# Performance work log

Hardware: AMD Instinct MI355X
Metric: run time of the kernel (lower is better)

## Reference

```python
import jax, jax.numpy as jnp
import numpy as np

DECAY = 0.99


def setup_inputs() -> dict:
    key = jax.random.key(0)
    k1, k2, k3, k4 = jax.random.split(key, 4)
    N, D, K = 65536, 256, 1024
    return {
        "masked_z_e_x": jax.random.normal(k1, (N, D), dtype=jnp.float32),
        "z_e_x": jax.random.normal(k2, (N, D), dtype=jnp.float32),
        "embedding": jax.random.normal(k3, (K, D), dtype=jnp.float32) * (1.0 / K),
        "ema_count": jnp.ones((K,), dtype=jnp.float32),
        "ema_w": jax.random.normal(k4, (K, D), dtype=jnp.float32) * (1.0 / K),
    }


def _vq_indices(x_flat, codebook):
    # distances[n,k] = ||x_n||^2 + ||c_k||^2 - 2 x_n . c_k  (addmm in torch)
    c_sqr = jnp.sum(codebook * codebook, axis=1)              # [K]
    x_sqr = jnp.sum(x_flat * x_flat, axis=1, keepdims=True)   # [N,1]
    dists = x_sqr + c_sqr - 2.0 * (x_flat @ codebook.T)       # [N,K]
    return jnp.argmin(dists, axis=1)                          # [N]


def reference(masked_z_e_x, z_e_x, embedding, ema_count, ema_w):
    K, D = embedding.shape
    x_flat = masked_z_e_x.reshape(-1, D)
    indices = _vq_indices(x_flat, embedding)                  # [N] int

    # straight-through quantized codes (value = gathered codes)
    z_q_x = embedding[indices].reshape(masked_z_e_x.shape)

    # EMA codebook update (training branch); one-hot matmul == segment sums
    z_flat = z_e_x.reshape(-1, D)
    counts = jax.ops.segment_sum(jnp.ones_like(indices, dtype=jnp.float32),
                                 indices, num_segments=K)     # [K]
    dw = jax.ops.segment_sum(z_flat, indices, num_segments=K) # [K,D]
    ema_count_new = DECAY * ema_count + (1.0 - DECAY) * counts
    ema_w_new = DECAY * ema_w + (1.0 - DECAY) * dw
    embedding_new = ema_w_new / ema_count_new[:, None]

    # re-gather from the updated (detached) codebook
    z_q_x_bar = embedding_new[indices].reshape(z_e_x.shape)
    return (z_q_x, z_q_x_bar, embedding_new, ema_count_new, ema_w_new)
```

## Files before the change

### kernel.cpp

```cpp
#include <hip/hip_runtime.h>

#define DDIM 256
#define KCODES 1024
#define MARGIN 2.0e-4f

typedef __attribute__((ext_vector_type(8))) short fragA;
typedef __attribute__((ext_vector_type(4))) float f32x4;

static __device__ __forceinline__ float4 ld4(const float* p) {
    return *reinterpret_cast<const float4*>(p);
}

static __device__ __forceinline__ ushort bf16_rne(float f) {
    unsigned bits = __float_as_uint(f);
    unsigned r = bits + 0x7FFFu + ((bits >> 16) & 1u);
    return (ushort)(r >> 16);
}

__global__ void split_sqnorm_kernel(const float* __restrict__ X, ushort* __restrict__ Xs,
                                    float* __restrict__ out, int nrows) {
    int row = blockIdx.x * 4 + (threadIdx.x >> 6);
    if (row >= nrows) return;
    int lane = threadIdx.x & 63;
    float4 v = reinterpret_cast<const float4*>(X + (size_t)row * DDIM)[lane];
    double s = (double)v.x * v.x + (double)v.y * v.y + (double)v.z * v.z + (double)v.w * v.w;
    #pragma unroll
    for (int off = 32; off > 0; off >>= 1) s += __shfl_down(s, off);
    if (lane == 0) out[row] = (float)s;

    float fv[4] = {v.x, v.y, v.z, v.w};
    ushort hb[4], lb[4];
    #pragma unroll
    for (int i = 0; i < 4; i++) {
        hb[i] = bf16_rne(fv[i]);
        float hf = __uint_as_float((unsigned)hb[i] << 16);
        lb[i] = bf16_rne(fv[i] - hf);
    }
    ushort4 hi = make_ushort4(hb[0], hb[1], hb[2], hb[3]);
    ushort4 lo = make_ushort4(lb[0], lb[1], lb[2], lb[3]);
    *reinterpret_cast<ushort4*>(Xs + (size_t)row * 512 + lane * 4) = hi;
    *reinterpret_cast<ushort4*>(Xs + (size_t)row * 512 + 256 + lane * 4) = lo;
}

__global__ __launch_bounds__(256) void argmin_mfma_kernel(
        const float* __restrict__ X, const ushort* __restrict__ Cs,
        float* __restrict__ xsq, const float* __restrict__ csq,
        int* __restrict__ indices, int* __restrict__ flag_cnt,
        int* __restrict__ flag_list, int* __restrict__ counts, int nrows_total) {
    __shared__ ushort clds[32 * 512];

    int tid = threadIdx.x;
    int w = tid >> 6;
    int l = tid & 63;
    int lm = l & 15;
    int lg = l >> 4;
    int row0 = blockIdx.x * 64;

    const float* xrowf = X + (size_t)(row0 + w * 16 + lm) * DDIM;
    fragA a_hi[8], a_lo[8];
    double dsum = 0.0;
    #pragma unroll
    for (int s = 0; s < 8; s++) {
        float4 v0 = ld4(xrowf + s * 32 + lg * 8);
        float4 v1 = ld4(xrowf + s * 32 + lg * 8 + 4);
        float f[8] = {v0.x, v0.y, v0.z, v0.w, v1.x, v1.y, v1.z, v1.w};
        fragA h, lo;
        #pragma unroll
        for (int j = 0; j < 8; j++) {
            dsum += (double)f[j] * f[j];
            ushort hb = bf16_rne(f[j]);
            float hf = __uint_as_float((unsigned)hb << 16);
            ushort lb = bf16_rne(f[j] - hf);
            h[j] = (short)hb;
            lo[j] = (short)lb;
        }
        a_hi[s] = h;
        a_lo[s] = lo;
    }
    dsum += __shfl_xor(dsum, 16);
    dsum += __shfl_xor(dsum, 32);
    float xsqf = (float)dsum;
    if (l < 16) xsq[row0 + w * 16 + l] = xsqf;
    float xs_r[4];
    #pragma unroll
    for (int r = 0; r < 4; r++) xs_r[r] = __shfl(xsqf, lg * 4 + r);

    float d1[4], d2[4];
    int k1[4];
    #pragma unroll
    for (int r = 0; r < 4; r++) { d1[r] = 3.0e38f; d2[r] = 3.0e38f; k1[r] = 0; }

    for (int kc = 0; kc < KCODES; kc += 32) {
        __syncthreads();
        #pragma unroll
        for (int it = 0; it < 8; it++) {
            int c = it * 256 + tid;
            int r = c >> 6, col = c & 63;
            int p = (col & 32) | ((col & 31) ^ (r & 7));
            *reinterpret_cast<float4*>(&clds[r * 512 + p * 8]) =
                *reinterpret_cast<const float4*>(Cs + (size_t)(kc + r) * 512 + col * 8);
        }
        __syncthreads();

        f32x4 acc[2];
        #pragma unroll
        for (int kt = 0; kt < 2; kt++) acc[kt] = (f32x4){0.f, 0.f, 0.f, 0.f};

        #pragma unroll
        for (int s = 0; s < 8; s++) {
            #pragma unroll
            for (int kt = 0; kt < 2; kt++) {
                int kl = kt * 16 + lm;
                int chi = (4 * s + lg) ^ (kl & 7);
                fragA bhi = *reinterpret_cast<const fragA*>(&clds[kl * 512 + chi * 8]);
                fragA blo = *reinterpret_cast<const fragA*>(&clds[kl * 512 + (32 + chi) * 8]);
                acc[kt] = __builtin_amdgcn_mfma_f32_16x16x32_bf16(a_hi[s], bhi, acc[kt], 0, 0, 0);
                acc[kt] = __builtin_amdgcn_mfma_f32_16x16x32_bf16(a_lo[s], bhi, acc[kt], 0, 0, 0);
                acc[kt] = __builtin_amdgcn_mfma_f32_16x16x32_bf16(a_hi[s], blo, acc[kt], 0, 0, 0);
            }
        }

        #pragma unroll
        for (int kt = 0; kt < 2; kt++) {
            int k = kc + kt * 16 + lm;
            float cs = csq[k];
            #pragma unroll
            for (int r = 0; r < 4; r++) {
                float dist = (xs_r[r] + cs) - 2.0f * acc[kt][r];
                if (dist < d1[r] || (dist == d1[r] && k < k1[r])) {
                    d2[r] = d1[r]; d1[r] = dist; k1[r] = k;
                } else if (dist < d2[r]) {
                    d2[r] = dist;
                }
            }
        }
    }

    #pragma unroll
    for (int r = 0; r < 4; r++) {
        float bd1 = d1[r], bd2 = d2[r];
        int bk1 = k1[r];
        #pragma unroll
        for (int m = 1; m < 16; m <<= 1) {
            float od1 = __shfl_xor(bd1, m);
            int ok1 = __shfl_xor(bk1, m);
            float od2 = __shfl_xor(bd2, m);
            if (od1 < bd1 || (od1 == bd1 && ok1 < bk1)) {
                bd2 = fminf(bd1, od2); bd1 = od1; bk1 = ok1;
            } else {
                bd2 = fminf(bd2, od1);
            }
        }
        if (lm == 0) {
            int row = row0 + w * 16 + lg * 4 + r;
            indices[row] = bk1;
            atomicAdd(&counts[bk1], 1);
            if (bd2 - bd1 < MARGIN) {
                int pos = atomicAdd(flag_cnt, 1);
                if (pos < nrows_total) flag_list[pos] = row;
            }
        }
    }
}

#define ECH 64
#define NKCH (KCODES / ECH)

__global__ __launch_bounds__(256) void exact_chunk_kernel(
        const float* __restrict__ X, const float* __restrict__ C,
        const float* __restrict__ xsq, const float* __restrict__ csq,
        const int* __restrict__ flag_cnt, const int* __restrict__ flag_list,
        unsigned long long* __restrict__ best64, int nrows_total) {
    __shared__ float xt[64][36];
    __shared__ float ct[64][36];
    __shared__ int rowidx[64];
    __shared__ float xsql[64];

    int cnt = *flag_cnt;
    if (cnt > nrows_total) cnt = nrows_total;
    if (cnt <= 0) return;
    int ntiles = (cnt + 63) >> 6;
    int nunits = ntiles * NKCH;

    int tid = threadIdx.x;
    int tx = tid & 15;
    int ty = tid >> 4;

    for (int u = blockIdx.x; u < nunits; u += gridDim.x) {
        int t = u >> 4;
        int kc = (u & 15) * ECH;
        int base = t * 64;

        __syncthreads();
        if (tid < 64) {
            int p = base + tid;
            int row = flag_list[p < cnt ? p : base];
            rowidx[tid] = row;
            xsql[tid] = xsq[row];
        }
        __syncthreads();

        float xs[4];
        #pragma unroll
        for (int i = 0; i < 4; i++) xs[i] = xsql[i * 16 + ty];

        float acc[4][4];
        #pragma unroll
        for (int i = 0; i < 4; i++)
            #pragma unroll
            for (int j = 0; j < 4; j++) acc[i][j] = 0.0f;

        for (int dt = 0; dt < DDIM; dt += 32) {
            __syncthreads();
            #pragma unroll
            for (int it = 0; it < 2; it++) {
                int e = it * 256 + tid;
                int r = e >> 3, c4 = e & 7;
                *reinterpret_cast<float4*>(&xt[r][c4 * 4]) =
                    ld4(X + (size_t)rowidx[r] * DDIM + dt + c4 * 4);
            }
            #pragma unroll
            for (int it = 0; it < 2; it++) {
                int e = it * 256 + tid;
                int r = e >> 3, c4 = e & 7;
                *reinterpret_cast<float4*>(&ct[r][c4 * 4]) =
                    ld4(C + (size_t)(kc + r) * DDIM + dt + c4 * 4);
            }
            __syncthreads();

            for (int d4 = 0; d4 < 32; d4 += 4) {
                float4 xv[4], cv[4];
                #pragma unroll
                for (int i = 0; i < 4; i++)
                    xv[i] = *reinterpret_cast<const float4*>(&xt[i * 16 + ty][d4]);
                #pragma unroll
                for (int j = 0; j < 4; j++)
                    cv[j] = *reinterpret_cast<const float4*>(&ct[j * 16 + tx][d4]);
                #pragma unroll
                for (int i = 0; i < 4; i++)
                    #pragma unroll
                    for (int j = 0; j < 4; j++) {
                        float a = acc[i][j];
                        a += xv[i].x * cv[j].x; a += xv[i].y * cv[j].y;
                        a += xv[i].z * cv[j].z; a += xv[i].w * cv[j].w;
                        acc[i][j] = a;
                    }
            }
        }

        float cs_r[4];
        #pragma unroll
        for (int j = 0; j < 4; j++) cs_r[j] = csq[kc + j * 16 + tx];

        #pragma unroll
        for (int i = 0; i < 4; i++) {
            float bd = 3.0e38f; int bk = 0;
            #pragma unroll
            for (int j = 0; j < 4; j++) {
                int kk = kc + j * 16 + tx;
                float tt = xs[i] + cs_r[j];
                float dist = tt - 2.0f * acc[i][j];
                if (dist < bd || (dist == bd && kk < bk)) { bd = dist; bk = kk; }
            }
            #pragma unroll
            for (int m = 1; m < 16; m <<= 1) {
                float od = __shfl_xor(bd, m);
                int ok = __shfl_xor(bk, m);
                if (od < bd || (od == bd && ok < bk)) { bd = od; bk = ok; }
            }
            if (tx == 0) {
                int p = base + i * 16 + ty;
                if (p < cnt) {
                    unsigned long long pk =
                        ((unsigned long long)__float_as_uint(bd) << 32) | (unsigned)bk;
                    atomicMin(&best64[p], pk);
                }
            }
        }
    }
}

__global__ void exact_finalize_kernel(const int* __restrict__ flag_cnt,
                                      const int* __restrict__ flag_list,
                                      const unsigned long long* __restrict__ best64,
                                      int* __restrict__ indices, int* __restrict__ counts,
                                      int nrows_total) {
    int cnt = *flag_cnt;
    if (cnt > nrows_total) cnt = nrows_total;
    for (int i = blockIdx.x * 256 + threadIdx.x; i < cnt; i += gridDim.x * 256) {
        int row = flag_list[i];
        int newk = (int)(best64[i] & 0xFFFFFFFFULL);
        int oldk = indices[row];
        if (newk != oldk) {
            indices[row] = newk;
            atomicAdd(&counts[oldk], -1);
            atomicAdd(&counts[newk], 1);
        }
    }
}

__global__ void prefix_kernel(const int* __restrict__ counts, int* __restrict__ offs,
                              int* __restrict__ cursor) {
    __shared__ int a[KCODES];
    int t = threadIdx.x;
    int v = counts[t];
    a[t] = v;
    __syncthreads();
    for (int s = 1; s < KCODES; s <<= 1) {
        int x = (t >= s) ? a[t - s] : 0;
        __syncthreads();
        a[t] += x;
        __syncthreads();
    }
    int excl = a[t] - v;
    offs[t] = excl;
    cursor[t] = excl;
}

__global__ void scatter_pos_kernel(const int* __restrict__ idx, int* __restrict__ cursor,
                                   int* __restrict__ sorted) {
    int i = blockIdx.x * 256 + threadIdx.x;
    int k = idx[i];
    int pos = atomicAdd(&cursor[k], 1);
    sorted[pos] = i;
}

__global__ __launch_bounds__(256) void segsum_ema_gather_kernel(
        const float* __restrict__ Z, const int* __restrict__ sorted,
        const int* __restrict__ offs, const int* __restrict__ counts,
        const float* __restrict__ ema_count, const float* __restrict__ ema_w,
        const float* __restrict__ emb,
        float* __restrict__ emb_new, float* __restrict__ cnt_new,
        float* __restrict__ w_new, float* __restrict__ zq, float* __restrict__ zqb) {
    int k = blockIdx.x;
    int t = threadIdx.x;
    int start = offs[k];
    int cnt = counts[k];

    float acc = 0.f;
    int j = 0;
    for (; j + 4 <= cnt; j += 4) {
        int r0 = sorted[start + j + 0];
        int r1 = sorted[start + j + 1];
        int r2 = sorted[start + j + 2];
        int r3 = sorted[start + j + 3];
        float v0 = Z[(size_t)r0 * DDIM + t];
        float v1 = Z[(size_t)r1 * DDIM + t];
        float v2 = Z[(size_t)r2 * DDIM + t];
        float v3 = Z[(size_t)r3 * DDIM + t];
        acc += v0; acc += v1; acc += v2; acc += v3;
    }
    for (; j < cnt; j++) {
        int r = sorted[start + j];
        acc += Z[(size_t)r * DDIM + t];
    }

    const float DEC = 0.99f;
    const float OMD = (float)(1.0 - 0.99);
    float cn = __fadd_rn(__fmul_rn(DEC, ema_count[k]), __fmul_rn(OMD, (float)cnt));
    float wn = __fadd_rn(__fmul_rn(DEC, ema_w[(size_t)k * DDIM + t]), __fmul_rn(OMD, acc));
    float en = __fdiv_rn(wn, cn);
    w_new[(size_t)k * DDIM + t] = wn;
    emb_new[(size_t)k * DDIM + t] = en;
    if (t == 0) cnt_new[k] = cn;

    float embk = emb[(size_t)k * DDIM + t];
    for (j = 0; j + 2 <= cnt; j += 2) {
        int r0 = sorted[start + j + 0];
        int r1 = sorted[start + j + 1];
        zq[(size_t)r0 * DDIM + t] = embk;
        zqb[(size_t)r0 * DDIM + t] = en;
        zq[(size_t)r1 * DDIM + t] = embk;
        zqb[(size_t)r1 * DDIM + t] = en;
    }
    for (; j < cnt; j++) {
        int r = sorted[start + j];
        zq[(size_t)r * DDIM + t] = embk;
        zqb[(size_t)r * DDIM + t] = en;
    }
}

extern "C" void kernel_launch(void* const* d_in, const int* in_sizes, int n_in,
                              void* d_out, int out_size, void* d_ws, size_t ws_size,
                              hipStream_t stream) {
    const float* x = (const float*)d_in[0];
    const float* z = (const float*)d_in[1];
    const float* emb = (const float*)d_in[2];
    const float* ema_count = (const float*)d_in[3];
    const float* ema_w = (const float*)d_in[4];

    const int N = in_sizes[0] / DDIM;
    const int K = in_sizes[3];

    float* out = (float*)d_out;
    float* zq = out;
    float* zqb = zq + (size_t)N * DDIM;
    float* emb_new = zqb + (size_t)N * DDIM;
    float* cnt_new = emb_new + (size_t)K * DDIM;
    float* w_new = cnt_new + K;

    char* wsb = (char*)d_ws;
    size_t off = 0;
    ushort* csplit = (ushort*)(wsb + off); off += (size_t)K * 512 * 2;
    float* xsq = (float*)(wsb + off); off += (size_t)N * 4;
    float* csq = (float*)(wsb + off); off += (size_t)K * 4;
    int* indices = (int*)(wsb + off); off += (size_t)N * 4;
    int* flag_list = (int*)(wsb + off); off += (size_t)N * 4;
    int* sorted = (int*)(wsb + off); off += (size_t)N * 4;
    int* offs = (int*)(wsb + off); off += (size_t)K * 4;
    int* counts = (int*)(wsb + off); off += (size_t)K * 4;
    int* cursor = (int*)(wsb + off); off += (size_t)K * 4;
    int* flag_cnt = (int*)(wsb + off); off += 16;
    unsigned long long* best64 = (unsigned long long*)(wsb + off); off += (size_t)N * 8;

    hipMemsetAsync(counts, 0, (size_t)K * 4 * 2 + 16, stream);
    hipMemsetAsync(best64, 0xFF, (size_t)N * 8, stream);
    split_sqnorm_kernel<<<K / 4, 256, 0, stream>>>(emb, csplit, csq, K);
    argmin_mfma_kernel<<<N / 64, 256, 0, stream>>>(x, csplit, xsq, csq,
                                                   indices, flag_cnt, flag_list, counts, N);
    exact_chunk_kernel<<<256, 256, 0, stream>>>(x, emb, xsq, csq,
                                                flag_cnt, flag_list, best64, N);
    exact_finalize_kernel<<<64, 256, 0, stream>>>(flag_cnt, flag_list, best64,
                                                  indices, counts, N);
    prefix_kernel<<<1, KCODES, 0, stream>>>(counts, offs, cursor);
    scatter_pos_kernel<<<N / 256, 256, 0, stream>>>(indices, cursor, sorted);
    segsum_ema_gather_kernel<<<K, 256, 0, stream>>>(z, sorted, offs, counts,
                                                    ema_count, ema_w, emb,
                                                    emb_new, cnt_new, w_new, zq, zqb);
}
```

Baseline: 273.2 us.

## Privatize code histogram in LDS, halve exact-chunk width, fuse finalize into prefix

The argmin kernel now accumulates per-block code counts in a shared-memory histogram and flushes them with one global atomic per nonzero bin, which cuts contention on global atomics. The exact re-check kernel now uses 32-code chunks and launches twice as many blocks, giving more parallel units when few rows are flagged. The exact-finalize step is folded into the single-block prefix kernel, removing one launch but running the fix-up loop on one workgroup.

```diff
diff --git a/kernel.cpp b/kernel.cpp
--- a/kernel.cpp
+++ b/kernel.cpp
@@ -48,6 +48,7 @@
         int* __restrict__ indices, int* __restrict__ flag_cnt,
         int* __restrict__ flag_list, int* __restrict__ counts, int nrows_total) {
     __shared__ ushort clds[32 * 512];
+    __shared__ int hist[KCODES];
 
     int tid = threadIdx.x;
     int w = tid >> 6;
@@ -55,6 +56,9 @@
     int lm = l & 15;
     int lg = l >> 4;
     int row0 = blockIdx.x * 64;
+
+    #pragma unroll
+    for (int i = 0; i < 4; i++) hist[tid + i * 256] = 0;
 
     const float* xrowf = X + (size_t)(row0 + w * 16 + lm) * DDIM;
     fragA a_hi[8], a_lo[8];
@@ -154,16 +158,23 @@
         if (lm == 0) {
             int row = row0 + w * 16 + lg * 4 + r;
             indices[row] = bk1;
-            atomicAdd(&counts[bk1], 1);
+            atomicAdd(&hist[bk1], 1);
             if (bd2 - bd1 < MARGIN) {
                 int pos = atomicAdd(flag_cnt, 1);
                 if (pos < nrows_total) flag_list[pos] = row;
             }
         }
     }
-}
-
-#define ECH 64
+
+    __syncthreads();
+    #pragma unroll
+    for (int i = 0; i < 4; i++) {
+        int v = hist[tid + i * 256];
+        if (v) atomicAdd(&counts[tid + i * 256], v);
+    }
+}
+
+#define ECH 32
 #define NKCH (KCODES / ECH)
 
 __global__ __launch_bounds__(256) void exact_chunk_kernel(
@@ -172,7 +183,7 @@
         const int* __restrict__ flag_cnt, const int* __restrict__ flag_list,
         unsigned long long* __restrict__ best64, int nrows_total) {
     __shared__ float xt[64][36];
-    __shared__ float ct[64][36];
+    __shared__ float ct[ECH][36];
     __shared__ int rowidx[64];
     __shared__ float xsql[64];
 
@@ -187,8 +198,8 @@
     int ty = tid >> 4;
 
     for (int u = blockIdx.x; u < nunits; u += gridDim.x) {
-        int t = u >> 4;
-        int kc = (u & 15) * ECH;
+        int t = u >> 5;
+        int kc = (u & 31) * ECH;
         int base = t * 64;
 
         __syncthreads();
@@ -204,11 +215,11 @@
         #pragma unroll
         for (int i = 0; i < 4; i++) xs[i] = xsql[i * 16 + ty];
 
-        float acc[4][4];
+        float acc[4][2];
         #pragma unroll
         for (int i = 0; i < 4; i++)
             #pragma unroll
-            for (int j = 0; j < 4; j++) acc[i][j] = 0.0f;
+            for (int j = 0; j < 2; j++) acc[i][j] = 0.0f;
 
         for (int dt = 0; dt < DDIM; dt += 32) {
             __syncthreads();
@@ -219,9 +230,8 @@
                 *reinterpret_cast<float4*>(&xt[r][c4 * 4]) =
                     ld4(X + (size_t)rowidx[r] * DDIM + dt + c4 * 4);
             }
-            #pragma unroll
-            for (int it = 0; it < 2; it++) {
-                int e = it * 256 + tid;
+            {
+                int e = tid;
                 int r = e >> 3, c4 = e & 7;
                 *reinterpret_cast<float4*>(&ct[r][c4 * 4]) =
                     ld4(C + (size_t)(kc + r) * DDIM + dt + c4 * 4);
@@ -229,17 +239,17 @@
             __syncthreads();
 
             for (int d4 = 0; d4 < 32; d4 += 4) {
-                float4 xv[4], cv[4];
+                float4 xv[4], cv[2];
                 #pragma unroll
                 for (int i = 0; i < 4; i++)
                     xv[i] = *reinterpret_cast<const float4*>(&xt[i * 16 + ty][d4]);
                 #pragma unroll
-                for (int j = 0; j < 4; j++)
+                for (int j = 0; j < 2; j++)
                     cv[j] = *reinterpret_cast<const float4*>(&ct[j * 16 + tx][d4]);
                 #pragma unroll
                 for (int i = 0; i < 4; i++)
                     #pragma unroll
-                    for (int j = 0; j < 4; j++) {
+                    for (int j = 0; j < 2; j++) {
                         float a = acc[i][j];
                         a += xv[i].x * cv[j].x; a += xv[i].y * cv[j].y;
                         a += xv[i].z * cv[j].z; a += xv[i].w * cv[j].w;
@@ -248,15 +258,15 @@
             }
         }
 
-        float cs_r[4];
-        #pragma unroll
-        for (int j = 0; j < 4; j++) cs_r[j] = csq[kc + j * 16 + tx];
+        float cs_r[2];
+        #pragma unroll
+        for (int j = 0; j < 2; j++) cs_r[j] = csq[kc + j * 16 + tx];
 
         #pragma unroll
         for (int i = 0; i < 4; i++) {
             float bd = 3.0e38f; int bk = 0;
             #pragma unroll
-            for (int j = 0; j < 4; j++) {
+            for (int j = 0; j < 2; j++) {
                 int kk = kc + j * 16 + tx;
                 float tt = xs[i] + cs_r[j];
                 float dist = tt - 2.0f * acc[i][j];
@@ -280,14 +290,17 @@
     }
 }
 
-__global__ void exact_finalize_kernel(const int* __restrict__ flag_cnt,
-                                      const int* __restrict__ flag_list,
-                                      const unsigned long long* __restrict__ best64,
-                                      int* __restrict__ indices, int* __restrict__ counts,
-                                      int nrows_total) {
+__global__ void prefix_kernel(const int* __restrict__ flag_cnt,
+                              const int* __restrict__ flag_list,
+                              const unsigned long long* __restrict__ best64,
+                              int* __restrict__ indices,
+                              int* __restrict__ counts, int* __restrict__ offs,
+                              int* __restrict__ cursor, int nrows_total) {
+    int t = threadIdx.x;
+
     int cnt = *flag_cnt;
     if (cnt > nrows_total) cnt = nrows_total;
-    for (int i = blockIdx.x * 256 + threadIdx.x; i < cnt; i += gridDim.x * 256) {
+    for (int i = t; i < cnt; i += KCODES) {
         int row = flag_list[i];
         int newk = (int)(best64[i] & 0xFFFFFFFFULL);
         int oldk = indices[row];
@@ -297,12 +310,10 @@
             atomicAdd(&counts[newk], 1);
         }
     }
-}
-
-__global__ void prefix_kernel(const int* __restrict__ counts, int* __restrict__ offs,
-                              int* __restrict__ cursor) {
+    __threadfence();
+    __syncthreads();
+
     __shared__ int a[KCODES];
-    int t = threadIdx.x;
     int v = counts[t];
     a[t] = v;
     __syncthreads();
@@ -418,11 +429,10 @@
     split_sqnorm_kernel<<<K / 4, 256, 0, stream>>>(emb, csplit, csq, K);
     argmin_mfma_kernel<<<N / 64, 256, 0, stream>>>(x, csplit, xsq, csq,
                                                    indices, flag_cnt, flag_list, counts, N);
-    exact_chunk_kernel<<<256, 256, 0, stream>>>(x, emb, xsq, csq,
+    exact_chunk_kernel<<<512, 256, 0, stream>>>(x, emb, xsq, csq,
                                                 flag_cnt, flag_list, best64, N);
-    exact_finalize_kernel<<<64, 256, 0, stream>>>(flag_cnt, flag_list, best64,
-                                                  indices, counts, N);
-    prefix_kernel<<<1, KCODES, 0, stream>>>(counts, offs, cursor);
+    prefix_kernel<<<1, KCODES, 0, stream>>>(flag_cnt, flag_list, best64, indices,
+                                            counts, offs, cursor, N);
     scatter_pos_kernel<<<N / 256, 256, 0, stream>>>(indices, cursor, sorted);
     segsum_ema_gather_kernel<<<K, 256, 0, stream>>>(z, sorted, offs, counts,
                                                     ema_count, ema_w, emb,
```

After: 267.8 us. 2.0% less time.
